# Kernel optimization log

Measured on AMD Instinct MI355X. Metric: run time of the kernel, lower is better.

The kernel has to match this reference:

```python
import jax, jax.numpy as jnp
import numpy as np

H = 8      # head_nums
D = 64     # head_planes
SCALE = D ** -0.5


def setup_inputs() -> dict:
    key = jax.random.key(0)
    ks = jax.random.split(key, 7)
    B, Nq, Nkv = 2, 2048, 2048
    Cq, Ck, I = 1024, 768, H * D
    return {
        "x": jax.random.normal(ks[0], (B, Nq, Cq), jnp.float32),
        "context": jax.random.normal(ks[1], (B, Nkv, Ck), jnp.float32),
        "Wq": jax.random.normal(ks[2], (Cq, I), jnp.float32) * (Cq ** -0.5),
        "Wk": jax.random.normal(ks[3], (Ck, I), jnp.float32) * (Ck ** -0.5),
        "Wv": jax.random.normal(ks[4], (Ck, I), jnp.float32) * (Ck ** -0.5),
        "Wo": jax.random.normal(ks[5], (I, Cq), jnp.float32) * (I ** -0.5),
        "bo": jnp.zeros((Cq,), jnp.float32),
    }


def reference(x, context, Wq, Wk, Wv, Wo, bo):
    B, Nq, _ = x.shape
    Nkv = context.shape[1]
    # projections (bias-free, as in to_q/to_k/to_v)
    q = (x @ Wq).reshape(B, Nq, H, D)        # b i h d
    k = (context @ Wk).reshape(B, Nkv, H, D)  # b j h d
    v = (context @ Wv).reshape(B, Nkv, H, D)
    # scaled dot-product attention, full [B,H,Nq,Nkv] scores as in original
    sim = jnp.einsum('bihd,bjhd->bhij', q, k) * SCALE
    attn = jax.nn.softmax(sim, axis=-1)
    out = jnp.einsum('bhij,bjhd->bihd', attn, v).reshape(B, Nq, H * D)
    # to_out linear (dropout_prob=0.0 -> identity)
    return out @ Wo + bo
```

## Files before the change

kernel.cpp:

```cpp
#include <hip/hip_runtime.h>
#include <hip/hip_bf16.h>

typedef __hip_bfloat16 bf16;
typedef __attribute__((ext_vector_type(8))) short short8;
typedef __attribute__((ext_vector_type(4))) short short4_;
typedef __attribute__((ext_vector_type(4))) float f32x4;

#define MFMA16(a, b, c) __builtin_amdgcn_mfma_f32_16x16x32_bf16((a), (b), (c), 0, 0, 0)

#define BATCH 2
#define NQ 2048
#define NKV 2048
#define HEADS 8
#define DHEAD 64
#define CQ 1024
#define CK 768
#define IDIM 512
#define SCALE 0.125f

__device__ __forceinline__ short8 ld8(const bf16* p) {
    return *(const short8*)p;
}

__device__ __forceinline__ void async_ld16(const bf16* g, bf16* l) {
    __builtin_amdgcn_global_load_lds((__attribute__((address_space(1))) const void*)g,
                                     (__attribute__((address_space(3))) void*)l,
                                     16, 0, 0);
}

__device__ __forceinline__ unsigned int pk2(float a, float b) {
    union { bf16 h[2]; unsigned int u; } x;
    x.h[0] = __float2bfloat16(a);
    x.h[1] = __float2bfloat16(b);
    return x.u;
}

__global__ __launch_bounds__(256) void prologue(
    const float* __restrict__ x, const float* __restrict__ ctx,
    const float* __restrict__ Wq, const float* __restrict__ Wk,
    const float* __restrict__ Wv, const float* __restrict__ Wo,
    bf16* __restrict__ Xb, bf16* __restrict__ Cb,
    bf16* __restrict__ WqT, bf16* __restrict__ WkT,
    bf16* __restrict__ WvT, bf16* __restrict__ WoT) {
    __shared__ float tile[64][65];
    const int t = threadIdx.x;
    const int bx = blockIdx.x;

    if (bx < 3584) {
        int idx = bx * 256 + t;
        const int NX8 = (4096 * 1024) / 8;
        const float4* srcp;
        bf16* dstp;
        if (idx < NX8) {
            srcp = (const float4*)x + (size_t)idx * 2;
            dstp = Xb + (size_t)idx * 8;
        } else {
            int j = idx - NX8;
            srcp = (const float4*)ctx + (size_t)j * 2;
            dstp = Cb + (size_t)j * 8;
        }
        float4 v0 = srcp[0], v1 = srcp[1];
        bf16 tmp[8] = {__float2bfloat16(v0.x), __float2bfloat16(v0.y),
                       __float2bfloat16(v0.z), __float2bfloat16(v0.w),
                       __float2bfloat16(v1.x), __float2bfloat16(v1.y),
                       __float2bfloat16(v1.z), __float2bfloat16(v1.w)};
        *(short8*)dstp = *(short8*)tmp;
        return;
    }

    int tb = bx - 3584;
    const float* src; bf16* dst; int R, C, ti;
    if (tb < 128)      { src = Wq; dst = WqT; R = 1024; C = 512;  ti = tb; }
    else if (tb < 224) { src = Wk; dst = WkT; R = 768;  C = 512;  ti = tb - 128; }
    else if (tb < 320) { src = Wv; dst = WvT; R = 768;  C = 512;  ti = tb - 224; }
    else               { src = Wo; dst = WoT; R = 512;  C = 1024; ti = tb - 320; }
    const int tilesC = C >> 6;
    const int tr = ti / tilesC, tc = ti - tr * tilesC;

    {
        int row = t >> 4;
        int c4 = (t & 15) * 4;
#pragma unroll
        for (int p = 0; p < 4; ++p) {
            float4 v = *(const float4*)&src[(size_t)(tr * 64 + p * 16 + row) * C + tc * 64 + c4];
            tile[p * 16 + row][c4 + 0] = v.x;
            tile[p * 16 + row][c4 + 1] = v.y;
            tile[p * 16 + row][c4 + 2] = v.z;
            tile[p * 16 + row][c4 + 3] = v.w;
        }
    }
    __syncthreads();
    {
        int oc = t >> 2;
        int r0 = (t & 3) * 16;
        bf16 tmp[16];
#pragma unroll
        for (int j = 0; j < 16; ++j)
            tmp[j] = __float2bfloat16(tile[r0 + j][oc]);
        bf16* dp = dst + (size_t)(tc * 64 + oc) * R + tr * 64 + r0;
        *(short8*)dp = *(short8*)&tmp[0];
        *(short8*)(dp + 8) = *(short8*)&tmp[8];
    }
}

__global__ __launch_bounds__(256) void qkv_gemm(
    const bf16* __restrict__ Xb, const bf16* __restrict__ Cb,
    const bf16* __restrict__ WqT, const bf16* __restrict__ WkT,
    const bf16* __restrict__ WvT,
    bf16* __restrict__ Qb, bf16* __restrict__ Kb, bf16* __restrict__ Vt) {
    __shared__ char SMEM[65536];
    bf16* At  = (bf16*)SMEM;
    bf16* Bts = (bf16*)(SMEM + 32768);
    bf16* Ep  = (bf16*)SMEM;

    const int z = blockIdx.z;
    const bf16* A  = (z == 0) ? Xb : Cb;
    const bf16* Bt = (z == 0) ? WqT : (z == 1) ? WkT : WvT;
    const int K = (z == 0) ? 1024 : 768;

    const int t = threadIdx.x;
    const int wave = t >> 6;
    const int lane = t & 63;
    const int n15 = lane & 15;
    const int quad = lane >> 4;
    const int wm = wave >> 1;
    const int wn = wave & 1;
    const int bm = blockIdx.x;
    const int bn = blockIdx.y;

    f32x4 acc[4][4] = {};

    const bf16* Ablk = A + (size_t)bm * 128 * K;
    const bf16* Bblk = Bt + (size_t)bn * 128 * K;

    int sr[4], sc[4];
#pragma unroll
    for (int i = 0; i < 4; ++i) {
        int g = i * 256 + t;
        sr[i] = g >> 3; sc[i] = ((g & 7) ^ (sr[i] & 7)) * 8;
    }

#pragma unroll
    for (int i = 0; i < 4; ++i)
        async_ld16(Ablk + sr[i] * K + sc[i], At + (i * 256 + t) * 8);
#pragma unroll
    for (int i = 0; i < 4; ++i)
        async_ld16(Bblk + sr[i] * K + sc[i], Bts + (i * 256 + t) * 8);
    __syncthreads();

    for (int k0 = 0; k0 < K; k0 += 64) {
        const int p = (k0 >> 6) & 1;
        if (k0 + 64 < K) {
            const int q = p ^ 1;
            const int kn = k0 + 64;
#pragma unroll
            for (int i = 0; i < 4; ++i)
                async_ld16(Ablk + sr[i] * K + kn + sc[i], At + q * 8192 + (i * 256 + t) * 8);
#pragma unroll
            for (int i = 0; i < 4; ++i)
                async_ld16(Bblk + sr[i] * K + kn + sc[i], Bts + q * 8192 + (i * 256 + t) * 8);
        }

#pragma unroll
        for (int kh = 0; kh < 2; ++kh) {
            short8 af[4], bfr[4];
#pragma unroll
            for (int mt = 0; mt < 4; ++mt) {
                int R = wm * 64 + mt * 16 + n15;
                af[mt] = ld8(At + p * 8192 + R * 64 + (((kh * 4 + quad) ^ (R & 7)) * 8));
            }
#pragma unroll
            for (int nt = 0; nt < 4; ++nt) {
                int R = wn * 64 + nt * 16 + n15;
                bfr[nt] = ld8(Bts + p * 8192 + R * 64 + (((kh * 4 + quad) ^ (R & 7)) * 8));
            }
#pragma unroll
            for (int mt = 0; mt < 4; ++mt)
#pragma unroll
                for (int nt = 0; nt < 4; ++nt)
                    acc[mt][nt] = MFMA16(af[mt], bfr[nt], acc[mt][nt]);
        }

        __syncthreads();
    }

    if (z < 2) {
#pragma unroll
        for (int mt = 0; mt < 4; ++mt)
#pragma unroll
            for (int nt = 0; nt < 4; ++nt) {
                int col = wn * 64 + nt * 16 + n15;
#pragma unroll
                for (int r = 0; r < 4; ++r) {
                    int row = wm * 64 + mt * 16 + quad * 4 + r;
                    Ep[row * 136 + col] = __float2bfloat16(acc[mt][nt][r]);
                }
            }
    } else {
#pragma unroll
        for (int mt = 0; mt < 4; ++mt)
#pragma unroll
            for (int nt = 0; nt < 4; ++nt) {
                int col = wn * 64 + nt * 16 + n15;
#pragma unroll
                for (int r = 0; r < 4; ++r) {
                    int row = wm * 64 + mt * 16 + quad * 4 + r;
                    Ep[col * 136 + row] = __float2bfloat16(acc[mt][nt][r]);
                }
            }
    }
    __syncthreads();

    bf16* C = (z == 0) ? Qb : (z == 1) ? Kb : Vt;
    if (z < 2) {
#pragma unroll
        for (int i = 0; i < 8; ++i) {
            int idx = i * 256 + t;
            int row = idx >> 4, seg = idx & 15;
            short8 v = ld8(&Ep[row * 136 + seg * 8]);
            *(short8*)&C[(size_t)(bm * 128 + row) * 512 + bn * 128 + seg * 8] = v;
        }
    } else {
        const int bb = bm >> 4;
#pragma unroll
        for (int i = 0; i < 8; ++i) {
            int idx = i * 256 + t;
            int col = idx >> 4, seg = idx & 15;
            int cg = bn * 128 + col;
            int hh = cg >> 6, dd = cg & 63;
            int jrow = (bm & 15) * 128 + seg * 8;
            short8 v = ld8(&Ep[col * 136 + seg * 8]);
            *(short8*)&C[(size_t)(((bb << 3) + hh) * 64 + dd) * 2048 + jrow] = v;
        }
    }
}

__global__ __launch_bounds__(256) void out_gemm(const bf16* __restrict__ A,
                                                const bf16* __restrict__ Bt,
                                                const float* __restrict__ bias,
                                                float* __restrict__ C) {
    const int K = 512, N = 1024;
    __shared__ char SMEM[65536];
    bf16* At  = (bf16*)SMEM;
    bf16* Bts = (bf16*)(SMEM + 32768);
    float* Ep = (float*)SMEM;

    const int t = threadIdx.x;
    const int wave = t >> 6;
    const int lane = t & 63;
    const int n15 = lane & 15;
    const int quad = lane >> 4;
    const int wm = wave >> 1;
    const int wn = wave & 1;
    const int bm = blockIdx.x;
    const int bn = blockIdx.y;

    f32x4 acc[4][4] = {};

    const bf16* Ablk = A + (size_t)bm * 128 * K;
    const bf16* Bblk = Bt + (size_t)bn * 128 * K;

    int sr[4], sc[4];
#pragma unroll
    for (int i = 0; i < 4; ++i) {
        int g = i * 256 + t;
        sr[i] = g >> 3; sc[i] = ((g & 7) ^ (sr[i] & 7)) * 8;
    }

#pragma unroll
    for (int i = 0; i < 4; ++i)
        async_ld16(Ablk + sr[i] * K + sc[i], At + (i * 256 + t) * 8);
#pragma unroll
    for (int i = 0; i < 4; ++i)
        async_ld16(Bblk + sr[i] * K + sc[i], Bts + (i * 256 + t) * 8);
    __syncthreads();

    for (int k0 = 0; k0 < K; k0 += 64) {
        const int p = (k0 >> 6) & 1;
        if (k0 + 64 < K) {
            const int q = p ^ 1;
            const int kn = k0 + 64;
#pragma unroll
            for (int i = 0; i < 4; ++i)
                async_ld16(Ablk + sr[i] * K + kn + sc[i], At + q * 8192 + (i * 256 + t) * 8);
#pragma unroll
            for (int i = 0; i < 4; ++i)
                async_ld16(Bblk + sr[i] * K + kn + sc[i], Bts + q * 8192 + (i * 256 + t) * 8);
        }

#pragma unroll
        for (int kh = 0; kh < 2; ++kh) {
            short8 af[4], bfr[4];
#pragma unroll
            for (int mt = 0; mt < 4; ++mt) {
                int R = wm * 64 + mt * 16 + n15;
                af[mt] = ld8(At + p * 8192 + R * 64 + (((kh * 4 + quad) ^ (R & 7)) * 8));
            }
#pragma unroll
            for (int nt = 0; nt < 4; ++nt) {
                int R = wn * 64 + nt * 16 + n15;
                bfr[nt] = ld8(Bts + p * 8192 + R * 64 + (((kh * 4 + quad) ^ (R & 7)) * 8));
            }
#pragma unroll
            for (int mt = 0; mt < 4; ++mt)
#pragma unroll
                for (int nt = 0; nt < 4; ++nt)
                    acc[mt][nt] = MFMA16(af[mt], bfr[nt], acc[mt][nt]);
        }

        __syncthreads();
    }

#pragma unroll
    for (int half = 0; half < 2; ++half) {
        if (wm == half) {
#pragma unroll
            for (int mt = 0; mt < 4; ++mt)
#pragma unroll
                for (int nt = 0; nt < 4; ++nt) {
                    int col = wn * 64 + nt * 16 + n15;
#pragma unroll
                    for (int r = 0; r < 4; ++r) {
                        int row = mt * 16 + quad * 4 + r;
                        Ep[row * 132 + col] = acc[mt][nt][r];
                    }
                }
        }
        __syncthreads();
#pragma unroll
        for (int i = 0; i < 8; ++i) {
            int f4 = i * 256 + t;
            int row = f4 >> 5;
            int c4 = (f4 & 31) * 4;
            float4 v = *(float4*)&Ep[row * 132 + c4];
            float4 bv = *(const float4*)&bias[bn * 128 + c4];
            v.x += bv.x; v.y += bv.y; v.z += bv.z; v.w += bv.w;
            *(float4*)&C[(size_t)(bm * 128 + half * 64 + row) * N + bn * 128 + c4] = v;
        }
        __syncthreads();
    }
}

__global__ __launch_bounds__(512, 4) void flash_attn(const bf16* __restrict__ Q,
                                                     const bf16* __restrict__ K,
                                                     const bf16* __restrict__ Vt,
                                                     bf16* __restrict__ O) {
    __shared__ bf16 Kt[2][2][64 * 64];
    __shared__ bf16 Vte[2][2][64 * 64];
    float* Oc = (float*)&Kt[0][0][0];
    float* Lc = (float*)((char*)&Kt[0][0][0] + 16384);
    bf16*  Pe = &Vte[0][0][0];

    const int t = threadIdx.x;
    const int wave = t >> 6;
    const int g = wave >> 1;
    const int khalf = wave & 1;
    const int lane = t & 63;
    const int n15 = lane & 15;
    const int quad = lane >> 4;

    const int L = blockIdx.x;
    const int bh = L & 15;
    const int b = bh >> 3, h = bh & 7;
    const int q0 = (L >> 4) * 64;
    const int qw = q0 + g * 16;

    const bf16* Qp = Q + ((size_t)(b * NQ + qw) * IDIM + h * DHEAD);
    const bf16* Kp = K + ((size_t)b * NKV * IDIM + h * DHEAD)
                       + (size_t)(khalf * 1024) * IDIM;
    const bf16* Vp = Vt + (size_t)((b * HEADS + h) * DHEAD) * NKV + khalf * 1024;

    short8 qa0 = ld8(Qp + n15 * IDIM + quad * 8);
    short8 qa1 = ld8(Qp + n15 * IDIM + 32 + quad * 8);

    const int s0 = g * 128 + lane;
    const int s1 = s0 + 64;
    const int r0 = s0 >> 3, c0 = (s0 & 7) ^ (r0 & 7);
    const int r1 = s1 >> 3, c1 = (s1 & 7) ^ (r1 & 7);
    const bf16* kg0 = Kp + r0 * IDIM + c0 * 8;
    const bf16* kg1 = Kp + r1 * IDIM + c1 * 8;
    const bf16* vg0 = Vp + (size_t)r0 * NKV + c0 * 8;
    const bf16* vg1 = Vp + (size_t)r1 * NKV + c1 * 8;

    f32x4 o[4] = {};
    float lsum = 0.f;
    const int sw = n15 & 7;
    const int qh = quad >> 1;
    const int qb = (quad & 1) << 2;

    async_ld16(kg0, &Kt[0][khalf][s0 * 8]);
    async_ld16(kg1, &Kt[0][khalf][s1 * 8]);
    async_ld16(vg0, &Vte[0][khalf][s0 * 8]);
    async_ld16(vg1, &Vte[0][khalf][s1 * 8]);

    for (int it = 0; it < 16; ++it) {
        const int cur = it & 1;
        asm volatile("s_waitcnt vmcnt(0)" ::: "memory");
        __syncthreads();
        if (it < 15) {
            const int kn = (it + 1) * 64;
            async_ld16(kg0 + (size_t)kn * IDIM, &Kt[cur ^ 1][khalf][s0 * 8]);
            async_ld16(kg1 + (size_t)kn * IDIM, &Kt[cur ^ 1][khalf][s1 * 8]);
            async_ld16(vg0 + kn, &Vte[cur ^ 1][khalf][s0 * 8]);
            async_ld16(vg1 + kn, &Vte[cur ^ 1][khalf][s1 * 8]);
        }

        f32x4 s[4] = {};
#pragma unroll
        for (int su = 0; su < 4; ++su) {
            const bf16* kr = &Kt[cur][khalf][(su * 16 + n15) * 64];
            short8 ka0 = ld8(kr + ((quad ^ sw) * 8));
            short8 ka1 = ld8(kr + (((4 + quad) ^ sw) * 8));
            s[su] = MFMA16(ka0, qa0, s[su]);
            s[su] = MFMA16(ka1, qa1, s[su]);
        }

        unsigned int w[4][2];
#pragma unroll
        for (int su = 0; su < 4; ++su) {
            float p0 = __expf(s[su][0] * SCALE);
            float p1 = __expf(s[su][1] * SCALE);
            float p2 = __expf(s[su][2] * SCALE);
            float p3 = __expf(s[su][3] * SCALE);
            lsum += (p0 + p1) + (p2 + p3);
            w[su][0] = pk2(p0, p1);
            w[su][1] = pk2(p2, p3);
        }
        union { short8 v; unsigned int u[4]; } pb0, pb1;
        pb0.u[0] = w[0][0]; pb0.u[1] = w[0][1]; pb0.u[2] = w[1][0]; pb0.u[3] = w[1][1];
        pb1.u[0] = w[2][0]; pb1.u[1] = w[2][1]; pb1.u[2] = w[3][0]; pb1.u[3] = w[3][1];

#pragma unroll
        for (int d4 = 0; d4 < 4; ++d4) {
            const bf16* vr = &Vte[cur][khalf][(d4 * 16 + n15) * 64];
            union { short8 v; short4_ hh[2]; } va0, va1;
            va0.hh[0] = *(const short4_*)(vr + (((qh    ) ^ sw) << 3) + qb);
            va0.hh[1] = *(const short4_*)(vr + (((qh | 2) ^ sw) << 3) + qb);
            va1.hh[0] = *(const short4_*)(vr + (((qh | 4) ^ sw) << 3) + qb);
            va1.hh[1] = *(const short4_*)(vr + (((qh | 6) ^ sw) << 3) + qb);
            o[d4] = MFMA16(va0.v, pb0.v, o[d4]);
            o[d4] = MFMA16(va1.v, pb1.v, o[d4]);
        }
    }

    lsum += __shfl_xor(lsum, 16, 64);
    lsum += __shfl_xor(lsum, 32, 64);

    __syncthreads();

    if (khalf == 1) {
#pragma unroll
        for (int d4 = 0; d4 < 4; ++d4)
#pragma unroll
            for (int r = 0; r < 4; ++r)
                Oc[(g * 64 + d4 * 16 + quad * 4 + r) * 16 + n15] = o[d4][r];
        if (quad == 0) Lc[g * 16 + n15] = lsum;
    }
    __syncthreads();
    if (khalf == 0) {
        float lt = lsum + Lc[g * 16 + n15];
        float inv = 1.0f / lt;
#pragma unroll
        for (int d4 = 0; d4 < 4; ++d4) {
            bf16 pk[4];
#pragma unroll
            for (int r = 0; r < 4; ++r) {
                float v = o[d4][r] + Oc[(g * 64 + d4 * 16 + quad * 4 + r) * 16 + n15];
                pk[r] = __float2bfloat16(v * inv);
            }
            *(uint2*)&Pe[g * (16 * 72) + n15 * 72 + d4 * 16 + quad * 4] = *(uint2*)pk;
        }
    }
    __syncthreads();

    {
        int ql = t >> 3, seg = t & 7;
        const bf16* src = &Pe[(ql >> 4) * (16 * 72) + (ql & 15) * 72 + seg * 8];
        short8 a0 = ld8(src);
        bf16* dst = O + ((size_t)(b * NQ + q0 + ql) * IDIM + h * DHEAD + seg * 8);
        *(short8*)dst = a0;
    }
}

extern "C" void kernel_launch(void* const* d_in, const int* in_sizes, int n_in,
                              void* d_out, int out_size, void* d_ws, size_t ws_size,
                              hipStream_t stream) {
    (void)in_sizes; (void)n_in; (void)out_size; (void)ws_size;

    const float* x   = (const float*)d_in[0];
    const float* ctx = (const float*)d_in[1];
    const float* Wq  = (const float*)d_in[2];
    const float* Wk  = (const float*)d_in[3];
    const float* Wv  = (const float*)d_in[4];
    const float* Wo  = (const float*)d_in[5];
    const float* bo  = (const float*)d_in[6];
    float* out = (float*)d_out;

    char* ws = (char*)d_ws;
    bf16* Xb  = (bf16*)(ws + 0);
    bf16* Cb  = (bf16*)(ws + 8388608);
    bf16* WqT = (bf16*)(ws + 14680064);
    bf16* WkT = (bf16*)(ws + 15728640);
    bf16* WvT = (bf16*)(ws + 16515072);
    bf16* WoT = (bf16*)(ws + 17301504);
    bf16* Qb  = (bf16*)(ws + 18350080);
    bf16* Kb  = (bf16*)(ws + 22544384);
    bf16* Vt  = (bf16*)(ws + 26738688);
    bf16* Ob  = (bf16*)(ws + 30932992);

    prologue<<<4032, 256, 0, stream>>>(x, ctx, Wq, Wk, Wv, Wo,
                                       Xb, Cb, WqT, WkT, WvT, WoT);

    qkv_gemm<<<dim3(32, 4, 3), 256, 0, stream>>>(Xb, Cb, WqT, WkT, WvT, Qb, Kb, Vt);

    flash_attn<<<512, 512, 0, stream>>>(Qb, Kb, Vt, Ob);

    out_gemm<<<dim3(32, 8), 256, 0, stream>>>(Ob, WoT, bo, out);
}
```

Measured before the change: 148.5 us.

## Fuse fp32-to-bf16 activation conversion into QKV GEMM A-tile loads

```diff
diff --git a/kernel.cpp b/kernel.cpp
--- a/kernel.cpp
+++ b/kernel.cpp
@@ -35,40 +35,23 @@
     return x.u;
 }
 
+__device__ __forceinline__ short8 cvt8(float4 v0, float4 v1) {
+    bf16 tmp[8] = {__float2bfloat16(v0.x), __float2bfloat16(v0.y),
+                   __float2bfloat16(v0.z), __float2bfloat16(v0.w),
+                   __float2bfloat16(v1.x), __float2bfloat16(v1.y),
+                   __float2bfloat16(v1.z), __float2bfloat16(v1.w)};
+    return *(short8*)tmp;
+}
+
 __global__ __launch_bounds__(256) void prologue(
-    const float* __restrict__ x, const float* __restrict__ ctx,
     const float* __restrict__ Wq, const float* __restrict__ Wk,
     const float* __restrict__ Wv, const float* __restrict__ Wo,
-    bf16* __restrict__ Xb, bf16* __restrict__ Cb,
     bf16* __restrict__ WqT, bf16* __restrict__ WkT,
     bf16* __restrict__ WvT, bf16* __restrict__ WoT) {
     __shared__ float tile[64][65];
     const int t = threadIdx.x;
-    const int bx = blockIdx.x;
-
-    if (bx < 3584) {
-        int idx = bx * 256 + t;
-        const int NX8 = (4096 * 1024) / 8;
-        const float4* srcp;
-        bf16* dstp;
-        if (idx < NX8) {
-            srcp = (const float4*)x + (size_t)idx * 2;
-            dstp = Xb + (size_t)idx * 8;
-        } else {
-            int j = idx - NX8;
-            srcp = (const float4*)ctx + (size_t)j * 2;
-            dstp = Cb + (size_t)j * 8;
-        }
-        float4 v0 = srcp[0], v1 = srcp[1];
-        bf16 tmp[8] = {__float2bfloat16(v0.x), __float2bfloat16(v0.y),
-                       __float2bfloat16(v0.z), __float2bfloat16(v0.w),
-                       __float2bfloat16(v1.x), __float2bfloat16(v1.y),
-                       __float2bfloat16(v1.z), __float2bfloat16(v1.w)};
-        *(short8*)dstp = *(short8*)tmp;
-        return;
-    }
-
-    int tb = bx - 3584;
+    const int tb = blockIdx.x;
+
     const float* src; bf16* dst; int R, C, ti;
     if (tb < 128)      { src = Wq; dst = WqT; R = 1024; C = 512;  ti = tb; }
     else if (tb < 224) { src = Wk; dst = WkT; R = 768;  C = 512;  ti = tb - 128; }
@@ -104,7 +87,7 @@
 }
 
 __global__ __launch_bounds__(256) void qkv_gemm(
-    const bf16* __restrict__ Xb, const bf16* __restrict__ Cb,
+    const float* __restrict__ x, const float* __restrict__ ctx,
     const bf16* __restrict__ WqT, const bf16* __restrict__ WkT,
     const bf16* __restrict__ WvT,
     bf16* __restrict__ Qb, bf16* __restrict__ Kb, bf16* __restrict__ Vt) {
@@ -114,7 +97,7 @@
     bf16* Ep  = (bf16*)SMEM;
 
     const int z = blockIdx.z;
-    const bf16* A  = (z == 0) ? Xb : Cb;
+    const float* A = (z == 0) ? x : ctx;
     const bf16* Bt = (z == 0) ? WqT : (z == 1) ? WkT : WvT;
     const int K = (z == 0) ? 1024 : 768;
 
@@ -130,7 +113,7 @@
 
     f32x4 acc[4][4] = {};
 
-    const bf16* Ablk = A + (size_t)bm * 128 * K;
+    const float* Ablk = A + (size_t)bm * 128 * K;
     const bf16* Bblk = Bt + (size_t)bn * 128 * K;
 
     int sr[4], sc[4];
@@ -141,8 +124,12 @@
     }
 
 #pragma unroll
-    for (int i = 0; i < 4; ++i)
-        async_ld16(Ablk + sr[i] * K + sc[i], At + (i * 256 + t) * 8);
+    for (int i = 0; i < 4; ++i) {
+        const float* ap = Ablk + (size_t)sr[i] * K + sc[i];
+        float4 v0 = *(const float4*)ap;
+        float4 v1 = *(const float4*)(ap + 4);
+        *(short8*)&At[(i * 256 + t) * 8] = cvt8(v0, v1);
+    }
 #pragma unroll
     for (int i = 0; i < 4; ++i)
         async_ld16(Bblk + sr[i] * K + sc[i], Bts + (i * 256 + t) * 8);
@@ -150,12 +137,17 @@
 
     for (int k0 = 0; k0 < K; k0 += 64) {
         const int p = (k0 >> 6) & 1;
-        if (k0 + 64 < K) {
-            const int q = p ^ 1;
+        const int q = p ^ 1;
+        const bool pre = (k0 + 64 < K);
+        float4 a0[4], a1[4];
+        if (pre) {
             const int kn = k0 + 64;
 #pragma unroll
-            for (int i = 0; i < 4; ++i)
-                async_ld16(Ablk + sr[i] * K + kn + sc[i], At + q * 8192 + (i * 256 + t) * 8);
+            for (int i = 0; i < 4; ++i) {
+                const float* ap = Ablk + (size_t)sr[i] * K + kn + sc[i];
+                a0[i] = *(const float4*)ap;
+                a1[i] = *(const float4*)(ap + 4);
+            }
 #pragma unroll
             for (int i = 0; i < 4; ++i)
                 async_ld16(Bblk + sr[i] * K + kn + sc[i], Bts + q * 8192 + (i * 256 + t) * 8);
@@ -179,6 +171,12 @@
 #pragma unroll
                 for (int nt = 0; nt < 4; ++nt)
                     acc[mt][nt] = MFMA16(af[mt], bfr[nt], acc[mt][nt]);
+        }
+
+        if (pre) {
+#pragma unroll
+            for (int i = 0; i < 4; ++i)
+                *(short8*)&At[q * 8192 + (i * 256 + t) * 8] = cvt8(a0[i], a1[i]);
         }
 
         __syncthreads();
@@ -497,21 +495,18 @@
     float* out = (float*)d_out;
 
     char* ws = (char*)d_ws;
-    bf16* Xb  = (bf16*)(ws + 0);
-    bf16* Cb  = (bf16*)(ws + 8388608);
-    bf16* WqT = (bf16*)(ws + 14680064);
-    bf16* WkT = (bf16*)(ws + 15728640);
-    bf16* WvT = (bf16*)(ws + 16515072);
-    bf16* WoT = (bf16*)(ws + 17301504);
-    bf16* Qb  = (bf16*)(ws + 18350080);
-    bf16* Kb  = (bf16*)(ws + 22544384);
-    bf16* Vt  = (bf16*)(ws + 26738688);
-    bf16* Ob  = (bf16*)(ws + 30932992);
-
-    prologue<<<4032, 256, 0, stream>>>(x, ctx, Wq, Wk, Wv, Wo,
-                                       Xb, Cb, WqT, WkT, WvT, WoT);
-
-    qkv_gemm<<<dim3(32, 4, 3), 256, 0, stream>>>(Xb, Cb, WqT, WkT, WvT, Qb, Kb, Vt);
+    bf16* WqT = (bf16*)(ws + 0);
+    bf16* WkT = (bf16*)(ws + 1048576);
+    bf16* WvT = (bf16*)(ws + 1835008);
+    bf16* WoT = (bf16*)(ws + 2621440);
+    bf16* Qb  = (bf16*)(ws + 3670016);
+    bf16* Kb  = (bf16*)(ws + 7864320);
+    bf16* Vt  = (bf16*)(ws + 12058624);
+    bf16* Ob  = (bf16*)(ws + 16252928);
+
+    prologue<<<448, 256, 0, stream>>>(Wq, Wk, Wv, Wo, WqT, WkT, WvT, WoT);
+
+    qkv_gemm<<<dim3(32, 4, 3), 256, 0, stream>>>(x, ctx, WqT, WkT, WvT, Qb, Kb, Vt);
 
     flash_attn<<<512, 512, 0, stream>>>(Qb, Kb, Vt, Ob);
 
```

After: 158.2 us. 6.5% more time.

## Load V fragments directly from global into registers, drop V shared-memory staging

Applied to the files above, without the earlier changes.

```diff
diff --git a/kernel.cpp b/kernel.cpp
--- a/kernel.cpp
+++ b/kernel.cpp
@@ -3,7 +3,6 @@
 
 typedef __hip_bfloat16 bf16;
 typedef __attribute__((ext_vector_type(8))) short short8;
-typedef __attribute__((ext_vector_type(4))) short short4_;
 typedef __attribute__((ext_vector_type(4))) float f32x4;
 
 #define MFMA16(a, b, c) __builtin_amdgcn_mfma_f32_16x16x32_bf16((a), (b), (c), 0, 0, 0)
@@ -346,10 +345,9 @@
                                                      const bf16* __restrict__ Vt,
                                                      bf16* __restrict__ O) {
     __shared__ bf16 Kt[2][2][64 * 64];
-    __shared__ bf16 Vte[2][2][64 * 64];
     float* Oc = (float*)&Kt[0][0][0];
     float* Lc = (float*)((char*)&Kt[0][0][0] + 16384);
-    bf16*  Pe = &Vte[0][0][0];
+    bf16*  Pe = (bf16*)((char*)&Kt[0][0][0] + 16640);
 
     const int t = threadIdx.x;
     const int wave = t >> 6;
@@ -379,33 +377,39 @@
     const int r1 = s1 >> 3, c1 = (s1 & 7) ^ (r1 & 7);
     const bf16* kg0 = Kp + r0 * IDIM + c0 * 8;
     const bf16* kg1 = Kp + r1 * IDIM + c1 * 8;
-    const bf16* vg0 = Vp + (size_t)r0 * NKV + c0 * 8;
-    const bf16* vg1 = Vp + (size_t)r1 * NKV + c1 * 8;
 
     f32x4 o[4] = {};
     float lsum = 0.f;
     const int sw = n15 & 7;
-    const int qh = quad >> 1;
-    const int qb = (quad & 1) << 2;
+
+    const bf16* vbase = Vp + (size_t)n15 * NKV + (quad << 2);
 
     async_ld16(kg0, &Kt[0][khalf][s0 * 8]);
     async_ld16(kg1, &Kt[0][khalf][s1 * 8]);
-    async_ld16(vg0, &Vte[0][khalf][s0 * 8]);
-    async_ld16(vg1, &Vte[0][khalf][s1 * 8]);
 
     for (int it = 0; it < 16; ++it) {
         const int cur = it & 1;
+        const int key0 = it * 64;
         asm volatile("s_waitcnt vmcnt(0)" ::: "memory");
         __syncthreads();
         if (it < 15) {
             const int kn = (it + 1) * 64;
             async_ld16(kg0 + (size_t)kn * IDIM, &Kt[cur ^ 1][khalf][s0 * 8]);
             async_ld16(kg1 + (size_t)kn * IDIM, &Kt[cur ^ 1][khalf][s1 * 8]);
-            async_ld16(vg0 + kn, &Vte[cur ^ 1][khalf][s0 * 8]);
-            async_ld16(vg1 + kn, &Vte[cur ^ 1][khalf][s1 * 8]);
+        }
+
+        uint2 vf[4][4];
+#pragma unroll
+        for (int d4 = 0; d4 < 4; ++d4) {
+            const bf16* vb = vbase + (size_t)(d4 * 16) * NKV + key0;
+            vf[d4][0] = *(const uint2*)vb;
+            vf[d4][1] = *(const uint2*)(vb + 16);
+            vf[d4][2] = *(const uint2*)(vb + 32);
+            vf[d4][3] = *(const uint2*)(vb + 48);
         }
 
         f32x4 s[4] = {};
+        __builtin_amdgcn_s_setprio(1);
 #pragma unroll
         for (int su = 0; su < 4; ++su) {
             const bf16* kr = &Kt[cur][khalf][(su * 16 + n15) * 64];
@@ -414,6 +418,7 @@
             s[su] = MFMA16(ka0, qa0, s[su]);
             s[su] = MFMA16(ka1, qa1, s[su]);
         }
+        __builtin_amdgcn_s_setprio(0);
 
         unsigned int w[4][2];
 #pragma unroll
@@ -430,17 +435,18 @@
         pb0.u[0] = w[0][0]; pb0.u[1] = w[0][1]; pb0.u[2] = w[1][0]; pb0.u[3] = w[1][1];
         pb1.u[0] = w[2][0]; pb1.u[1] = w[2][1]; pb1.u[2] = w[3][0]; pb1.u[3] = w[3][1];
 
+        __builtin_amdgcn_s_setprio(1);
 #pragma unroll
         for (int d4 = 0; d4 < 4; ++d4) {
-            const bf16* vr = &Vte[cur][khalf][(d4 * 16 + n15) * 64];
-            union { short8 v; short4_ hh[2]; } va0, va1;
-            va0.hh[0] = *(const short4_*)(vr + (((qh    ) ^ sw) << 3) + qb);
-            va0.hh[1] = *(const short4_*)(vr + (((qh | 2) ^ sw) << 3) + qb);
-            va1.hh[0] = *(const short4_*)(vr + (((qh | 4) ^ sw) << 3) + qb);
-            va1.hh[1] = *(const short4_*)(vr + (((qh | 6) ^ sw) << 3) + qb);
+            union { short8 v; uint2 hh[2]; } va0, va1;
+            va0.hh[0] = vf[d4][0];
+            va0.hh[1] = vf[d4][1];
+            va1.hh[0] = vf[d4][2];
+            va1.hh[1] = vf[d4][3];
             o[d4] = MFMA16(va0.v, pb0.v, o[d4]);
             o[d4] = MFMA16(va1.v, pb1.v, o[d4]);
         }
+        __builtin_amdgcn_s_setprio(0);
     }
 
     lsum += __shfl_xor(lsum, 16, 64);
```

Result: slower. 239.6 us (+61.3%).

## Process two query tiles per wave in flash attention with half the waves

Applied to the files above, without the earlier changes.

```diff
diff --git a/kernel.cpp b/kernel.cpp
--- a/kernel.cpp
+++ b/kernel.cpp
@@ -341,7 +341,7 @@
     }
 }
 
-__global__ __launch_bounds__(512, 4) void flash_attn(const bf16* __restrict__ Q,
+__global__ __launch_bounds__(256, 2) void flash_attn(const bf16* __restrict__ Q,
                                                      const bf16* __restrict__ K,
                                                      const bf16* __restrict__ Vt,
                                                      bf16* __restrict__ O) {
@@ -349,7 +349,7 @@
     __shared__ bf16 Vte[2][2][64 * 64];
     float* Oc = (float*)&Kt[0][0][0];
     float* Lc = (float*)((char*)&Kt[0][0][0] + 16384);
-    bf16*  Pe = &Vte[0][0][0];
+    bf16*  Pe = (bf16*)((char*)&Kt[0][0][0] + 16640);
 
     const int t = threadIdx.x;
     const int wave = t >> 6;
@@ -363,35 +363,39 @@
     const int bh = L & 15;
     const int b = bh >> 3, h = bh & 7;
     const int q0 = (L >> 4) * 64;
-    const int qw = q0 + g * 16;
+    const int qw = q0 + g * 32;
 
     const bf16* Qp = Q + ((size_t)(b * NQ + qw) * IDIM + h * DHEAD);
     const bf16* Kp = K + ((size_t)b * NKV * IDIM + h * DHEAD)
                        + (size_t)(khalf * 1024) * IDIM;
     const bf16* Vp = Vt + (size_t)((b * HEADS + h) * DHEAD) * NKV + khalf * 1024;
 
-    short8 qa0 = ld8(Qp + n15 * IDIM + quad * 8);
-    short8 qa1 = ld8(Qp + n15 * IDIM + 32 + quad * 8);
-
-    const int s0 = g * 128 + lane;
-    const int s1 = s0 + 64;
-    const int r0 = s0 >> 3, c0 = (s0 & 7) ^ (r0 & 7);
-    const int r1 = s1 >> 3, c1 = (s1 & 7) ^ (r1 & 7);
-    const bf16* kg0 = Kp + r0 * IDIM + c0 * 8;
-    const bf16* kg1 = Kp + r1 * IDIM + c1 * 8;
-    const bf16* vg0 = Vp + (size_t)r0 * NKV + c0 * 8;
-    const bf16* vg1 = Vp + (size_t)r1 * NKV + c1 * 8;
-
-    f32x4 o[4] = {};
-    float lsum = 0.f;
+    short8 qaA0 = ld8(Qp + n15 * IDIM + quad * 8);
+    short8 qaA1 = ld8(Qp + n15 * IDIM + 32 + quad * 8);
+    short8 qaB0 = ld8(Qp + (size_t)(16 + n15) * IDIM + quad * 8);
+    short8 qaB1 = ld8(Qp + (size_t)(16 + n15) * IDIM + 32 + quad * 8);
+
+    int ss[4];
+    const bf16 *kg[4], *vg[4];
+#pragma unroll
+    for (int i = 0; i < 4; ++i) {
+        ss[i] = i * 128 + g * 64 + lane;
+        int r = ss[i] >> 3, c = (ss[i] & 7) ^ (r & 7);
+        kg[i] = Kp + r * IDIM + c * 8;
+        vg[i] = Vp + (size_t)r * NKV + c * 8;
+    }
+
+    f32x4 oA[4] = {}, oB[4] = {};
+    float lsumA = 0.f, lsumB = 0.f;
     const int sw = n15 & 7;
     const int qh = quad >> 1;
     const int qb = (quad & 1) << 2;
 
-    async_ld16(kg0, &Kt[0][khalf][s0 * 8]);
-    async_ld16(kg1, &Kt[0][khalf][s1 * 8]);
-    async_ld16(vg0, &Vte[0][khalf][s0 * 8]);
-    async_ld16(vg1, &Vte[0][khalf][s1 * 8]);
+#pragma unroll
+    for (int i = 0; i < 4; ++i) {
+        async_ld16(kg[i], &Kt[0][khalf][ss[i] * 8]);
+        async_ld16(vg[i], &Vte[0][khalf][ss[i] * 8]);
+    }
 
     for (int it = 0; it < 16; ++it) {
         const int cur = it & 1;
@@ -399,36 +403,48 @@
         __syncthreads();
         if (it < 15) {
             const int kn = (it + 1) * 64;
-            async_ld16(kg0 + (size_t)kn * IDIM, &Kt[cur ^ 1][khalf][s0 * 8]);
-            async_ld16(kg1 + (size_t)kn * IDIM, &Kt[cur ^ 1][khalf][s1 * 8]);
-            async_ld16(vg0 + kn, &Vte[cur ^ 1][khalf][s0 * 8]);
-            async_ld16(vg1 + kn, &Vte[cur ^ 1][khalf][s1 * 8]);
-        }
-
-        f32x4 s[4] = {};
+#pragma unroll
+            for (int i = 0; i < 4; ++i) {
+                async_ld16(kg[i] + (size_t)kn * IDIM, &Kt[cur ^ 1][khalf][ss[i] * 8]);
+                async_ld16(vg[i] + kn, &Vte[cur ^ 1][khalf][ss[i] * 8]);
+            }
+        }
+
+        f32x4 sA[4] = {}, sB[4] = {};
 #pragma unroll
         for (int su = 0; su < 4; ++su) {
             const bf16* kr = &Kt[cur][khalf][(su * 16 + n15) * 64];
             short8 ka0 = ld8(kr + ((quad ^ sw) * 8));
             short8 ka1 = ld8(kr + (((4 + quad) ^ sw) * 8));
-            s[su] = MFMA16(ka0, qa0, s[su]);
-            s[su] = MFMA16(ka1, qa1, s[su]);
-        }
-
-        unsigned int w[4][2];
+            sA[su] = MFMA16(ka0, qaA0, sA[su]);
+            sA[su] = MFMA16(ka1, qaA1, sA[su]);
+            sB[su] = MFMA16(ka0, qaB0, sB[su]);
+            sB[su] = MFMA16(ka1, qaB1, sB[su]);
+        }
+
+        unsigned int wA[4][2], wB[4][2];
 #pragma unroll
         for (int su = 0; su < 4; ++su) {
-            float p0 = __expf(s[su][0] * SCALE);
-            float p1 = __expf(s[su][1] * SCALE);
-            float p2 = __expf(s[su][2] * SCALE);
-            float p3 = __expf(s[su][3] * SCALE);
-            lsum += (p0 + p1) + (p2 + p3);
-            w[su][0] = pk2(p0, p1);
-            w[su][1] = pk2(p2, p3);
-        }
-        union { short8 v; unsigned int u[4]; } pb0, pb1;
-        pb0.u[0] = w[0][0]; pb0.u[1] = w[0][1]; pb0.u[2] = w[1][0]; pb0.u[3] = w[1][1];
-        pb1.u[0] = w[2][0]; pb1.u[1] = w[2][1]; pb1.u[2] = w[3][0]; pb1.u[3] = w[3][1];
+            float a0 = __expf(sA[su][0] * SCALE);
+            float a1 = __expf(sA[su][1] * SCALE);
+            float a2 = __expf(sA[su][2] * SCALE);
+            float a3 = __expf(sA[su][3] * SCALE);
+            lsumA += (a0 + a1) + (a2 + a3);
+            wA[su][0] = pk2(a0, a1);
+            wA[su][1] = pk2(a2, a3);
+            float b0 = __expf(sB[su][0] * SCALE);
+            float b1 = __expf(sB[su][1] * SCALE);
+            float b2 = __expf(sB[su][2] * SCALE);
+            float b3 = __expf(sB[su][3] * SCALE);
+            lsumB += (b0 + b1) + (b2 + b3);
+            wB[su][0] = pk2(b0, b1);
+            wB[su][1] = pk2(b2, b3);
+        }
+        union { short8 v; unsigned int u[4]; } pb0A, pb1A, pb0B, pb1B;
+        pb0A.u[0] = wA[0][0]; pb0A.u[1] = wA[0][1]; pb0A.u[2] = wA[1][0]; pb0A.u[3] = wA[1][1];
+        pb1A.u[0] = wA[2][0]; pb1A.u[1] = wA[2][1]; pb1A.u[2] = wA[3][0]; pb1A.u[3] = wA[3][1];
+        pb0B.u[0] = wB[0][0]; pb0B.u[1] = wB[0][1]; pb0B.u[2] = wB[1][0]; pb0B.u[3] = wB[1][1];
+        pb1B.u[0] = wB[2][0]; pb1B.u[1] = wB[2][1]; pb1B.u[2] = wB[3][0]; pb1B.u[3] = wB[3][1];
 
 #pragma unroll
         for (int d4 = 0; d4 < 4; ++d4) {
@@ -438,13 +454,17 @@
             va0.hh[1] = *(const short4_*)(vr + (((qh | 2) ^ sw) << 3) + qb);
             va1.hh[0] = *(const short4_*)(vr + (((qh | 4) ^ sw) << 3) + qb);
             va1.hh[1] = *(const short4_*)(vr + (((qh | 6) ^ sw) << 3) + qb);
-            o[d4] = MFMA16(va0.v, pb0.v, o[d4]);
-            o[d4] = MFMA16(va1.v, pb1.v, o[d4]);
-        }
-    }
-
-    lsum += __shfl_xor(lsum, 16, 64);
-    lsum += __shfl_xor(lsum, 32, 64);
+            oA[d4] = MFMA16(va0.v, pb0A.v, oA[d4]);
+            oA[d4] = MFMA16(va1.v, pb1A.v, oA[d4]);
+            oB[d4] = MFMA16(va0.v, pb0B.v, oB[d4]);
+            oB[d4] = MFMA16(va1.v, pb1B.v, oB[d4]);
+        }
+    }
+
+    lsumA += __shfl_xor(lsumA, 16, 64);
+    lsumA += __shfl_xor(lsumA, 32, 64);
+    lsumB += __shfl_xor(lsumB, 16, 64);
+    lsumB += __shfl_xor(lsumB, 32, 64);
 
     __syncthreads();
 
@@ -452,31 +472,40 @@
 #pragma unroll
         for (int d4 = 0; d4 < 4; ++d4)
 #pragma unroll
-            for (int r = 0; r < 4; ++r)
-                Oc[(g * 64 + d4 * 16 + quad * 4 + r) * 16 + n15] = o[d4][r];
-        if (quad == 0) Lc[g * 16 + n15] = lsum;
+            for (int r = 0; r < 4; ++r) {
+                int drow = g * 64 + d4 * 16 + quad * 4 + r;
+                Oc[drow * 32 + n15]      = oA[d4][r];
+                Oc[drow * 32 + 16 + n15] = oB[d4][r];
+            }
+        if (quad == 0) {
+            Lc[g * 32 + n15]      = lsumA;
+            Lc[g * 32 + 16 + n15] = lsumB;
+        }
     }
     __syncthreads();
     if (khalf == 0) {
-        float lt = lsum + Lc[g * 16 + n15];
-        float inv = 1.0f / lt;
+        float invA = 1.0f / (lsumA + Lc[g * 32 + n15]);
+        float invB = 1.0f / (lsumB + Lc[g * 32 + 16 + n15]);
 #pragma unroll
         for (int d4 = 0; d4 < 4; ++d4) {
-            bf16 pk[4];
+            bf16 pkA[4], pkB[4];
 #pragma unroll
             for (int r = 0; r < 4; ++r) {
-                float v = o[d4][r] + Oc[(g * 64 + d4 * 16 + quad * 4 + r) * 16 + n15];
-                pk[r] = __float2bfloat16(v * inv);
-            }
-            *(uint2*)&Pe[g * (16 * 72) + n15 * 72 + d4 * 16 + quad * 4] = *(uint2*)pk;
-        }
-    }
-    __syncthreads();
-
-    {
-        int ql = t >> 3, seg = t & 7;
-        const bf16* src = &Pe[(ql >> 4) * (16 * 72) + (ql & 15) * 72 + seg * 8];
-        short8 a0 = ld8(src);
+                int drow = g * 64 + d4 * 16 + quad * 4 + r;
+                pkA[r] = __float2bfloat16((oA[d4][r] + Oc[drow * 32 + n15]) * invA);
+                pkB[r] = __float2bfloat16((oB[d4][r] + Oc[drow * 32 + 16 + n15]) * invB);
+            }
+            *(uint2*)&Pe[(g * 32 + n15) * 72 + d4 * 16 + quad * 4]      = *(uint2*)pkA;
+            *(uint2*)&Pe[(g * 32 + 16 + n15) * 72 + d4 * 16 + quad * 4] = *(uint2*)pkB;
+        }
+    }
+    __syncthreads();
+
+#pragma unroll
+    for (int i = 0; i < 2; ++i) {
+        int idx = i * 256 + t;
+        int ql = idx >> 3, seg = idx & 7;
+        short8 a0 = ld8(&Pe[ql * 72 + seg * 8]);
         bf16* dst = O + ((size_t)(b * NQ + q0 + ql) * IDIM + h * DHEAD + seg * 8);
         *(short8*)dst = a0;
     }
@@ -513,7 +542,7 @@
 
     qkv_gemm<<<dim3(32, 4, 3), 256, 0, stream>>>(Xb, Cb, WqT, WkT, WvT, Qb, Kb, Vt);
 
-    flash_attn<<<512, 512, 0, stream>>>(Qb, Kb, Vt, Ob);
+    flash_attn<<<512, 256, 0, stream>>>(Qb, Kb, Vt, Ob);
 
     out_gemm<<<dim3(32, 8), 256, 0, stream>>>(Ob, WoT, bo, out);
 }
```

Result: no change. 148.6 us (+0.0%).
